# Performance work log

Hardware: AMD Instinct MI355X
Metric: run time of the kernel (lower is better)

Reference implementation:

```python
import jax, jax.numpy as jnp
import numpy as np

B, N = 256, 65536


def setup_inputs() -> dict:
    key = jax.random.key(0)
    k1, k2, k3, k4 = jax.random.split(key, 4)
    # x scaled so that v_new occasionally exceeds v_peak=30 and the WTA path fires
    x = jax.random.normal(k1, (B, N), dtype=jnp.float32) * 60.0
    v = jax.random.normal(k2, (B, N), dtype=jnp.float32)
    i = jax.random.normal(k3, (B, N), dtype=jnp.float32)
    w = jax.random.normal(k4, (B, N), dtype=jnp.float32)
    return {"x": x, "v": v, "i": i, "w": w}


def reference(x, v, i, w):
    # Default LIFAdExParameters from __init__
    TAU_SYN_INV = 0.5
    TAU_MEM_INV = 0.5
    TAU_ADAPT_INV = 0.5
    V_REST = 0.0
    V_RESET = 0.0
    V_TH = 1.0
    V_PEAK = 30.0
    A_PARAM = 0.0
    B_PARAM = 0.0
    DELTA_T = 1.0
    INHIBITION = -5.0

    # AdEx LIF elementwise step
    i_new = i + TAU_SYN_INV * (x - i)
    exp_term = DELTA_T * jnp.exp((v - V_TH) / DELTA_T)
    v_new = v + TAU_MEM_INV * (-(v - V_REST) + exp_term + i_new - w)
    w_new = w + TAU_ADAPT_INV * (A_PARAM * (v - V_REST) - w)
    z = (v_new >= V_PEAK).astype(v_new.dtype)
    v_before = v_new  # membrane potential before reset, used to pick winner
    v_new = jnp.where(z > 0, V_RESET, v_new)
    w_new = jnp.where(z > 0, w_new + B_PARAM, w_new)

    # Winner-take-all lateral inhibition on batch row 0 (as in original forward)
    spiked0 = z[0] > 0
    any_spike0 = jnp.any(spiked0)
    winner = jnp.argmax(jnp.where(spiked0, v_before[0], -jnp.inf))
    inhibit = any_spike0 & (jnp.arange(z.shape[1]) != winner)  # [N]
    v_new = v_new.at[0].set(jnp.where(inhibit, INHIBITION, v_new[0]))
    w_new = w_new.at[0].set(jnp.where(inhibit, 0.0, w_new[0]))

    # (z, new_state) -> return z plus the new state tensors (v, i, w)
    return z, v_new, i_new, w_new
```

## Files before the change

### kernel.cpp

```cpp
#include <hip/hip_runtime.h>
#include <cstdint>

static constexpr int B_DIM = 256;
static constexpr int N_DIM = 65536;
static constexpr int BN = B_DIM * N_DIM;
static constexpr int VEC = BN / 4;
static constexpr int ROW0_VEC = N_DIM / 4;

__global__ __launch_bounds__(256) void lif_main(
    const float4* __restrict__ x, const float4* __restrict__ v,
    const float4* __restrict__ cur, const float4* __restrict__ w,
    float4* __restrict__ z_out, float4* __restrict__ v_out,
    float4* __restrict__ i_out, float4* __restrict__ w_out,
    unsigned long long* __restrict__ ws_key)
{
    const int t = blockIdx.x * blockDim.x + threadIdx.x;
    if (t >= VEC) return;

    const float4 xv = x[t];
    const float4 vv = v[t];
    const float4 iv = cur[t];
    const float4 wv = w[t];

    float4 zo, vo, io, wo;
    const float* xp = reinterpret_cast<const float*>(&xv);
    const float* vp = reinterpret_cast<const float*>(&vv);
    const float* ip = reinterpret_cast<const float*>(&iv);
    const float* wp = reinterpret_cast<const float*>(&wv);
    float* zq = reinterpret_cast<float*>(&zo);
    float* vq = reinterpret_cast<float*>(&vo);
    float* iq = reinterpret_cast<float*>(&io);
    float* wq = reinterpret_cast<float*>(&wo);

    const bool row0 = (t < ROW0_VEC);
    unsigned long long key = 0ull;

    #pragma unroll
    for (int k = 0; k < 4; ++k) {
        const float X = xp[k];
        const float V = vp[k];
        const float I = ip[k];
        const float W = wp[k];

        const float i_new = I + 0.5f * (X - I);
        const float e     = expf(V - 1.0f);
        float v_new       = V + 0.5f * (-V + e + i_new - W);
        const float w_new = 0.5f * W;

        const bool spike  = (v_new >= 30.0f);
        const float v_before = v_new;
        if (spike) v_new = 0.0f;

        zq[k] = spike ? 1.0f : 0.0f;
        vq[k] = v_new;
        iq[k] = i_new;
        wq[k] = w_new;

        if (row0 && spike) {
            const unsigned vb  = __float_as_uint(v_before);
            const unsigned idx = (unsigned)(t * 4 + k);
            const unsigned long long cand =
                ((unsigned long long)vb << 32) | (unsigned long long)(~idx);
            key = (cand > key) ? cand : key;
        }
    }

    z_out[t] = zo;
    v_out[t] = vo;
    i_out[t] = io;
    w_out[t] = wo;

    if (row0) {
        #pragma unroll
        for (int off = 32; off > 0; off >>= 1) {
            unsigned long long other = __shfl_down(key, off, 64);
            key = (other > key) ? other : key;
        }
        if ((threadIdx.x & 63) == 0 && key != 0ull) {
            atomicMax(ws_key, key);
        }
    }
}

__global__ __launch_bounds__(256) void lif_inhibit(
    float* __restrict__ v_row0, float* __restrict__ w_row0,
    const unsigned long long* __restrict__ ws_key)
{
    const unsigned long long key = *ws_key;
    if (key == 0ull) return;
    const unsigned winner = ~(unsigned)(key & 0xFFFFFFFFull);
    const int n = blockIdx.x * blockDim.x + threadIdx.x;
    if (n < N_DIM && (unsigned)n != winner) {
        v_row0[n] = -5.0f;
        w_row0[n] = 0.0f;
    }
}

extern "C" void kernel_launch(void* const* d_in, const int* in_sizes, int n_in,
                              void* d_out, int out_size, void* d_ws, size_t ws_size,
                              hipStream_t stream) {
    const float* x   = (const float*)d_in[0];
    const float* v   = (const float*)d_in[1];
    const float* cur = (const float*)d_in[2];
    const float* w   = (const float*)d_in[3];
    float* out = (float*)d_out;

    float* z_out = out;
    float* v_out = out + (size_t)BN;
    float* i_out = out + 2ull * BN;
    float* w_out = out + 3ull * BN;

    unsigned long long* key = (unsigned long long*)d_ws;
    hipMemsetAsync(d_ws, 0, sizeof(unsigned long long), stream);

    lif_main<<<VEC / 256, 256, 0, stream>>>(
        (const float4*)x, (const float4*)v, (const float4*)cur, (const float4*)w,
        (float4*)z_out, (float4*)v_out, (float4*)i_out, (float4*)w_out, key);

    lif_inhibit<<<N_DIM / 256, 256, 0, stream>>>(v_out, w_out, key);
}
```

Measured before the change: 444.0 us.

## Fuse WTA inhibition into main kernel via last-block ticket and nontemporal I/O

Removes the separate inhibition kernel launch. The last row-0 block to finish, found through an atomic ticket counter, reads the winner key and rewrites row 0 of v and w itself. All loads and stores also switch to nontemporal builtins on ext_vector types, to avoid polluting the cache on a purely streaming workload. The row-0 fixup is now serialized in a single block, and it relies on threadfence ordering for the cross-block read of v_out and w_out.

```diff
diff --git a/kernel.cpp b/kernel.cpp
--- a/kernel.cpp
+++ b/kernel.cpp
@@ -6,41 +6,39 @@
 static constexpr int BN = B_DIM * N_DIM;
 static constexpr int VEC = BN / 4;
 static constexpr int ROW0_VEC = N_DIM / 4;
+static constexpr int TPB = 256;
+static constexpr int NROW0_BLK = ROW0_VEC / TPB;
 
-__global__ __launch_bounds__(256) void lif_main(
-    const float4* __restrict__ x, const float4* __restrict__ v,
-    const float4* __restrict__ cur, const float4* __restrict__ w,
-    float4* __restrict__ z_out, float4* __restrict__ v_out,
-    float4* __restrict__ i_out, float4* __restrict__ w_out,
-    unsigned long long* __restrict__ ws_key)
+typedef float floatx4 __attribute__((ext_vector_type(4)));
+
+__global__ __launch_bounds__(TPB) void lif_fused(
+    const floatx4* __restrict__ x, const floatx4* __restrict__ v,
+    const floatx4* __restrict__ cur, const floatx4* __restrict__ w,
+    floatx4* __restrict__ z_out, floatx4* __restrict__ v_out,
+    floatx4* __restrict__ i_out, floatx4* __restrict__ w_out,
+    unsigned long long* __restrict__ ws_key,
+    unsigned int* __restrict__ ws_cnt)
 {
-    const int t = blockIdx.x * blockDim.x + threadIdx.x;
-    if (t >= VEC) return;
+    const int tid = threadIdx.x;
+    const int bid = blockIdx.x;
+    const int t = bid * TPB + tid;
 
-    const float4 xv = x[t];
-    const float4 vv = v[t];
-    const float4 iv = cur[t];
-    const float4 wv = w[t];
+    const floatx4 xv = __builtin_nontemporal_load(&x[t]);
+    const floatx4 vv = __builtin_nontemporal_load(&v[t]);
+    const floatx4 iv = __builtin_nontemporal_load(&cur[t]);
+    const floatx4 wv = __builtin_nontemporal_load(&w[t]);
 
-    float4 zo, vo, io, wo;
-    const float* xp = reinterpret_cast<const float*>(&xv);
-    const float* vp = reinterpret_cast<const float*>(&vv);
-    const float* ip = reinterpret_cast<const float*>(&iv);
-    const float* wp = reinterpret_cast<const float*>(&wv);
-    float* zq = reinterpret_cast<float*>(&zo);
-    float* vq = reinterpret_cast<float*>(&vo);
-    float* iq = reinterpret_cast<float*>(&io);
-    float* wq = reinterpret_cast<float*>(&wo);
+    floatx4 zo, vo, io, wo;
 
-    const bool row0 = (t < ROW0_VEC);
+    const bool row0 = (bid < NROW0_BLK);
     unsigned long long key = 0ull;
 
     #pragma unroll
     for (int k = 0; k < 4; ++k) {
-        const float X = xp[k];
-        const float V = vp[k];
-        const float I = ip[k];
-        const float W = wp[k];
+        const float X = xv[k];
+        const float V = vv[k];
+        const float I = iv[k];
+        const float W = wv[k];
 
         const float i_new = I + 0.5f * (X - I);
         const float e     = expf(V - 1.0f);
@@ -51,10 +49,10 @@
         const float v_before = v_new;
         if (spike) v_new = 0.0f;
 
-        zq[k] = spike ? 1.0f : 0.0f;
-        vq[k] = v_new;
-        iq[k] = i_new;
-        wq[k] = w_new;
+        zo[k] = spike ? 1.0f : 0.0f;
+        vo[k] = v_new;
+        io[k] = i_new;
+        wo[k] = w_new;
 
         if (row0 && spike) {
             const unsigned vb  = __float_as_uint(v_before);
@@ -65,34 +63,57 @@
         }
     }
 
-    z_out[t] = zo;
-    v_out[t] = vo;
-    i_out[t] = io;
-    w_out[t] = wo;
+    __builtin_nontemporal_store(zo, &z_out[t]);
+    __builtin_nontemporal_store(vo, &v_out[t]);
+    __builtin_nontemporal_store(io, &i_out[t]);
+    __builtin_nontemporal_store(wo, &w_out[t]);
 
-    if (row0) {
-        #pragma unroll
-        for (int off = 32; off > 0; off >>= 1) {
-            unsigned long long other = __shfl_down(key, off, 64);
-            key = (other > key) ? other : key;
+    if (!row0) return;
+
+    #pragma unroll
+    for (int off = 32; off > 0; off >>= 1) {
+        const unsigned long long other = __shfl_down(key, off, 64);
+        key = (other > key) ? other : key;
+    }
+    if ((tid & 63) == 0 && key != 0ull) {
+        atomicMax(ws_key, key);
+    }
+
+    __threadfence();
+    __syncthreads();
+
+    __shared__ unsigned int ticket;
+    if (tid == 0) ticket = atomicAdd(ws_cnt, 1u);
+    __syncthreads();
+
+    if (ticket == NROW0_BLK - 1) {
+        __threadfence();
+
+        __shared__ unsigned long long skey;
+        if (tid == 0) skey = atomicMax(ws_key, 0ull);
+        __syncthreads();
+        const unsigned long long kk = skey;
+        if (kk == 0ull) return;
+
+        const unsigned winner = ~(unsigned)(kk & 0xFFFFFFFFull);
+        float* v0 = reinterpret_cast<float*>(v_out);
+        float* w0 = reinterpret_cast<float*>(w_out);
+
+        const float vwin = v0[winner];
+        const float wwin = w0[winner];
+        __syncthreads();
+
+        const floatx4 m5 = {-5.0f, -5.0f, -5.0f, -5.0f};
+        const floatx4 z4 = {0.0f, 0.0f, 0.0f, 0.0f};
+        for (int i2 = tid; i2 < ROW0_VEC; i2 += TPB) {
+            v_out[i2] = m5;
+            w_out[i2] = z4;
         }
-        if ((threadIdx.x & 63) == 0 && key != 0ull) {
-            atomicMax(ws_key, key);
+        __syncthreads();
+        if (tid == 0) {
+            v0[winner] = vwin;
+            w0[winner] = wwin;
         }
-    }
-}
-
-__global__ __launch_bounds__(256) void lif_inhibit(
-    float* __restrict__ v_row0, float* __restrict__ w_row0,
-    const unsigned long long* __restrict__ ws_key)
-{
-    const unsigned long long key = *ws_key;
-    if (key == 0ull) return;
-    const unsigned winner = ~(unsigned)(key & 0xFFFFFFFFull);
-    const int n = blockIdx.x * blockDim.x + threadIdx.x;
-    if (n < N_DIM && (unsigned)n != winner) {
-        v_row0[n] = -5.0f;
-        w_row0[n] = 0.0f;
     }
 }
 
@@ -111,11 +132,10 @@
     float* w_out = out + 3ull * BN;
 
     unsigned long long* key = (unsigned long long*)d_ws;
-    hipMemsetAsync(d_ws, 0, sizeof(unsigned long long), stream);
+    unsigned int* cnt = (unsigned int*)((char*)d_ws + 8);
+    (void)hipMemsetAsync(d_ws, 0, 16, stream);
 
-    lif_main<<<VEC / 256, 256, 0, stream>>>(
-        (const float4*)x, (const float4*)v, (const float4*)cur, (const float4*)w,
-        (float4*)z_out, (float4*)v_out, (float4*)i_out, (float4*)w_out, key);
-
-    lif_inhibit<<<N_DIM / 256, 256, 0, stream>>>(v_out, w_out, key);
+    lif_fused<<<VEC / TPB, TPB, 0, stream>>>(
+        (const floatx4*)x, (const floatx4*)v, (const floatx4*)cur, (const floatx4*)w,
+        (floatx4*)z_out, (floatx4*)v_out, (floatx4*)i_out, (floatx4*)w_out, key, cnt);
 }
```

Measured after the change: 445.0 us. About the same (+0.2%).
